# Kernel tuning notes

Hardware: AMD Instinct MI355X
Metric: run time of the kernel (lower is better)

Reference implementation:

```python
import jax, jax.numpy as jnp
import numpy as np

BATCH, E = 4096, 8
DIMS = [512, 1024, 1024, 512]


def setup_inputs() -> dict:
    key = jax.random.key(0)
    ks = jax.random.split(key, 8)
    inp = {
        'weight_blend': jax.random.uniform(ks[0], (BATCH, E), dtype=jnp.float32),
        'x': jax.random.normal(ks[1], (BATCH, DIMS[0]), dtype=jnp.float32),
    }
    for i in range(3):
        inp[f'W{i}'] = jax.random.normal(ks[2 + i], (E, DIMS[i + 1], DIMS[i]), dtype=jnp.float32)
        inp[f'B{i}'] = jnp.zeros((E, DIMS[i + 1]), dtype=jnp.float32)
    return inp


def _blended_layer(weight_blend, x, W, B):
    # Fused form of: weight = sum_e blend[b,e]*W[e]; y = bmm(weight, x) + sum_e blend[b,e]*B[e]
    # Computed as sum_e blend_e * (W_e @ x) without materializing (batch,out,in).
    y = jnp.einsum('eoi,bi->beo', W, x)          # per-expert GEMM, (B,E,out)
    y = jnp.einsum('be,beo->bo', weight_blend, y)  # blend combine
    return y + weight_blend @ B                   # blended bias (B,out)


def reference(weight_blend, x, W0, B0, W1, B1, W2, B2):
    # Dropout with keep_prob=0.0 is identity in eval mode; activations: elu, elu, linear.
    h = jax.nn.elu(_blended_layer(weight_blend, x, W0, B0))
    h = jax.nn.elu(_blended_layer(weight_blend, h, W1, B1))
    out = _blended_layer(weight_blend, h, W2, B2)
    return out
```

## Files before the change

kernel.cpp:

```cpp
#include <hip/hip_runtime.h>
#include <cstdint>
#include <cstddef>

typedef __bf16 bf16x8 __attribute__((ext_vector_type(8)));
typedef float f32x4 __attribute__((ext_vector_type(4)));
typedef unsigned short u16;
typedef unsigned short u16x8 __attribute__((ext_vector_type(8)));

#define BATCH 4096
#define NE 8

__device__ __forceinline__ u16 f2bf(float f) {
  union { float f; uint32_t u; } v; v.f = f;
  uint32_t u = v.u;
  u += 0x7fffu + ((u >> 16) & 1u);
  return (u16)(u >> 16);
}

__device__ __forceinline__ void cast8(const float* src, u16* dst) {
  const float4* p = (const float4*)src;
  float4 a = p[0], b = p[1];
  u16x8 o;
  o[0] = f2bf(a.x); o[1] = f2bf(a.y); o[2] = f2bf(a.z); o[3] = f2bf(a.w);
  o[4] = f2bf(b.x); o[5] = f2bf(b.y); o[6] = f2bf(b.z); o[7] = f2bf(b.w);
  *(u16x8*)dst = o;
}

__device__ __forceinline__ void conv_w_chunk(const float* __restrict__ W,
                                             u16* __restrict__ Bt,
                                             int N, int K0, int chunk) {
  int per_row = K0 >> 3;
  int rid = chunk / per_row;
  int i0 = (chunk - rid * per_row) << 3;
  int e = rid / N;
  int o = rid - e * N;
  cast8(W + (size_t)rid * K0 + i0,
        Bt + (size_t)o * ((size_t)NE * K0) + (size_t)e * K0 + i0);
}

__global__ void prep_kernel(const float* __restrict__ x,
                            const float* __restrict__ W0,
                            const float* __restrict__ W1,
                            const float* __restrict__ W2,
                            u16* __restrict__ h0, u16* __restrict__ Bt0,
                            u16* __restrict__ Bt1, u16* __restrict__ Bt2) {
  int t = blockIdx.x * blockDim.x + threadIdx.x;
  const int C0 = BATCH * 512 / 8;
  const int C1 = C0 + NE * 1024 * 512 / 8;
  const int C2 = C1 + NE * 1024 * 1024 / 8;
  if (t < C0) {
    cast8(x + (size_t)t * 8, h0 + (size_t)t * 8);
  } else if (t < C1) {
    conv_w_chunk(W0, Bt0, 1024, 512, t - C0);
  } else if (t < C2) {
    conv_w_chunk(W1, Bt1, 1024, 1024, t - C1);
  } else {
    conv_w_chunk(W2, Bt2, 512, 1024, t - C2);
  }
}

template<int SLICES, bool ELU_ACT, bool OUT_BF16>
__global__ void combine_kernel(const float* __restrict__ P,
                               const float* __restrict__ blend,
                               const float* __restrict__ Bias,
                               void* __restrict__ outp, int N) {
  int t = blockIdx.x * blockDim.x + threadIdx.x;
  int per_row = N >> 3;
  int b = t / per_row;
  int i0 = (t - b * per_row) << 3;
  const size_t slice = (size_t)BATCH * N;
  float v[8] = {0, 0, 0, 0, 0, 0, 0, 0};
  #pragma unroll
  for (int s = 0; s < SLICES; ++s) {
    const float4* p = (const float4*)(P + s * slice + (size_t)b * N + i0);
    float4 pa = p[0], pb = p[1];
    v[0] += pa.x; v[1] += pa.y; v[2] += pa.z; v[3] += pa.w;
    v[4] += pb.x; v[5] += pb.y; v[6] += pb.z; v[7] += pb.w;
  }
  const float4* blp = (const float4*)(blend + b * NE);
  float4 u0 = blp[0], u1 = blp[1];
  float bl[8] = {u0.x, u0.y, u0.z, u0.w, u1.x, u1.y, u1.z, u1.w};
  #pragma unroll
  for (int e = 0; e < NE; ++e) {
    const float4* bp = (const float4*)(Bias + (size_t)e * N + i0);
    float4 ba = bp[0], bb = bp[1];
    float bv[8] = {ba.x, ba.y, ba.z, ba.w, bb.x, bb.y, bb.z, bb.w};
    #pragma unroll
    for (int j = 0; j < 8; ++j) v[j] += bl[e] * bv[j];
  }
  if (ELU_ACT) {
    #pragma unroll
    for (int j = 0; j < 8; ++j) v[j] = v[j] > 0.f ? v[j] : expm1f(v[j]);
  }
  if (OUT_BF16) {
    u16x8 o;
    #pragma unroll
    for (int j = 0; j < 8; ++j) o[j] = f2bf(v[j]);
    *(u16x8*)((u16*)outp + (size_t)b * N + i0) = o;
  } else {
    float4* op = (float4*)((float*)outp + (size_t)b * N + i0);
    op[0] = (float4){v[0], v[1], v[2], v[3]};
    op[1] = (float4){v[4], v[5], v[6], v[7]};
  }
}

#define GL2LDS(g, l) __builtin_amdgcn_global_load_lds( \
    (__attribute__((address_space(1))) void*)(g),      \
    (__attribute__((address_space(3))) void*)(l), 16, 0, 0)

template<int K0, int NEXP>
__global__ __launch_bounds__(256, 2)
void gemm_hb_kernel(const u16* __restrict__ h, const u16* __restrict__ Bt,
                    const float* __restrict__ blend, float* __restrict__ P, int N) {
  __shared__ __align__(16) u16 Hs[128 * 32];
  __shared__ __align__(16) u16 Bs[128 * 32];
  __shared__ float bls[128 * NE];

  const int tid  = threadIdx.x;
  const int w    = tid >> 6, lane = tid & 63;
  const int wm   = w >> 1,   wn   = w & 1;
  const int lrow = lane & 15, quad = lane >> 4;

  const int row0 = blockIdx.x * 128;
  const int col0 = blockIdx.y * 128;
  const int EK = K0 * NE;
  const int e0 = blockIdx.z * NEXP;

  ((float4*)bls)[tid] = ((const float4*)(blend + (size_t)row0 * NE))[tid];

  const u16* gH0 = h + (size_t)(row0 + (tid >> 2)) * K0 + ((tid & 3) << 3);
  const u16* gH1 = gH0 + (size_t)64 * K0;
  const u16* gB0 = Bt + (size_t)(col0 + (tid >> 2)) * EK + (size_t)e0 * K0 + ((tid & 3) << 3);
  const u16* gB1 = gB0 + (size_t)64 * EK;
  u16* lH0 = &Hs[tid * 8];
  u16* lH1 = &Hs[tid * 8 + 2048];
  u16* lB0 = &Bs[tid * 8];
  u16* lB1 = &Bs[tid * 8 + 2048];

  const u16* fH[4];
  const u16* fB[4];
  #pragma unroll
  for (int i = 0; i < 4; ++i) {
    fH[i] = &Hs[(wm * 64 + i * 16 + lrow) * 32 + quad * 8];
    fB[i] = &Bs[(wn * 64 + i * 16 + lrow) * 32 + quad * 8];
  }

  f32x4 acc[4][4];
  #pragma unroll
  for (int i = 0; i < 4; ++i)
    #pragma unroll
    for (int j = 0; j < 4; ++j) acc[i][j] = (f32x4){0.f, 0.f, 0.f, 0.f};

  #pragma unroll
  for (int e = 0; e < NEXP; ++e) {
    f32x4 acc2[4][4];
    #pragma unroll
    for (int i = 0; i < 4; ++i)
      #pragma unroll
      for (int j = 0; j < 4; ++j) acc2[i][j] = (f32x4){0.f, 0.f, 0.f, 0.f};

    const u16* pH0 = gH0;
    const u16* pH1 = gH1;
    const u16* pB0 = gB0 + (size_t)e * K0;
    const u16* pB1 = gB1 + (size_t)e * K0;

    for (int it = 0; it < K0 / 32; ++it) {
      GL2LDS(pH0, lH0);
      GL2LDS(pH1, lH1);
      GL2LDS(pB0, lB0);
      GL2LDS(pB1, lB1);
      pH0 += 32; pH1 += 32; pB0 += 32; pB1 += 32;
      __syncthreads();

      bf16x8 hf[4], bfr[4];
      #pragma unroll
      for (int i = 0; i < 4; ++i) hf[i] = *(const bf16x8*)fH[i];
      #pragma unroll
      for (int j = 0; j < 4; ++j) bfr[j] = *(const bf16x8*)fB[j];
      #pragma unroll
      for (int i = 0; i < 4; ++i)
        #pragma unroll
        for (int j = 0; j < 4; ++j)
          acc2[i][j] = __builtin_amdgcn_mfma_f32_16x16x32_bf16(hf[i], bfr[j], acc2[i][j], 0, 0, 0);
      __syncthreads();
    }

    #pragma unroll
    for (int mt = 0; mt < 4; ++mt) {
      float bl[4];
      #pragma unroll
      for (int r = 0; r < 4; ++r)
        bl[r] = bls[(wm * 64 + mt * 16 + quad * 4 + r) * NE + (e0 + e)];
      #pragma unroll
      for (int nt = 0; nt < 4; ++nt)
        #pragma unroll
        for (int r = 0; r < 4; ++r)
          acc[mt][nt][r] += bl[r] * acc2[mt][nt][r];
    }
  }

  float* Ps = P + (size_t)blockIdx.z * ((size_t)BATCH * N);
  #pragma unroll
  for (int mt = 0; mt < 4; ++mt) {
    #pragma unroll
    for (int r = 0; r < 4; ++r) {
      int row = row0 + wm * 64 + mt * 16 + quad * 4 + r;
      #pragma unroll
      for (int nt = 0; nt < 4; ++nt) {
        int col = col0 + wn * 64 + nt * 16 + lrow;
        Ps[(size_t)row * N + col] = acc[mt][nt][r];
      }
    }
  }
}

extern "C" void kernel_launch(void* const* d_in, const int* in_sizes, int n_in,
                              void* d_out, int out_size, void* d_ws, size_t ws_size,
                              hipStream_t stream) {
  const float* blend = (const float*)d_in[0];
  const float* x  = (const float*)d_in[1];
  const float* W0 = (const float*)d_in[2];
  const float* B0 = (const float*)d_in[3];
  const float* W1 = (const float*)d_in[4];
  const float* B1 = (const float*)d_in[5];
  const float* W2 = (const float*)d_in[6];
  const float* B2 = (const float*)d_in[7];
  float* out = (float*)d_out;

  char* ws = (char*)d_ws;
  u16*   hA  = (u16*)ws;
  u16*   h1  = (u16*)(ws + 8388608);
  u16*   Bt0 = (u16*)(ws + 16777216);
  u16*   Bt1 = (u16*)(ws + 25165824);
  u16*   Bt2 = (u16*)(ws + 41943040);
  float* P   = (float*)(ws + 50331648);

  prep_kernel<<<9216, 256, 0, stream>>>(x, W0, W1, W2, hA, Bt0, Bt1, Bt2);

  gemm_hb_kernel<512, 2><<<dim3(32, 8, 4), 256, 0, stream>>>(hA, Bt0, blend, P, 1024);
  combine_kernel<4, true, true><<<2048, 256, 0, stream>>>(P, blend, B0, h1, 1024);

  gemm_hb_kernel<1024, 2><<<dim3(32, 8, 4), 256, 0, stream>>>(h1, Bt1, blend, P, 1024);
  combine_kernel<4, true, true><<<2048, 256, 0, stream>>>(P, blend, B1, hA, 1024);

  gemm_hb_kernel<1024, 1><<<dim3(32, 4, 8), 256, 0, stream>>>(hA, Bt2, blend, P, 512);
  combine_kernel<8, false, false><<<1024, 256, 0, stream>>>(P, blend, B2, out, 512);
}
```

Baseline: 355.4 us.

## Store per-expert GEMM outputs in bf16 and apply blend in combine kernel

```diff
diff --git a/kernel.cpp b/kernel.cpp
--- a/kernel.cpp
+++ b/kernel.cpp
@@ -15,6 +15,11 @@
   uint32_t u = v.u;
   u += 0x7fffu + ((u >> 16) & 1u);
   return (u16)(u >> 16);
+}
+
+__device__ __forceinline__ float bf2f(u16 u) {
+  union { uint32_t u; float f; } v; v.u = ((uint32_t)u) << 16;
+  return v.f;
 }
 
 __device__ __forceinline__ void cast8(const float* src, u16* dst) {
@@ -59,27 +64,26 @@
   }
 }
 
-template<int SLICES, bool ELU_ACT, bool OUT_BF16>
-__global__ void combine_kernel(const float* __restrict__ P,
-                               const float* __restrict__ blend,
-                               const float* __restrict__ Bias,
-                               void* __restrict__ outp, int N) {
+template<bool ELU_ACT, bool OUT_BF16>
+__global__ void combine8_kernel(const u16* __restrict__ P,
+                                const float* __restrict__ blend,
+                                const float* __restrict__ Bias,
+                                void* __restrict__ outp, int N) {
   int t = blockIdx.x * blockDim.x + threadIdx.x;
   int per_row = N >> 3;
   int b = t / per_row;
   int i0 = (t - b * per_row) << 3;
   const size_t slice = (size_t)BATCH * N;
-  float v[8] = {0, 0, 0, 0, 0, 0, 0, 0};
-  #pragma unroll
-  for (int s = 0; s < SLICES; ++s) {
-    const float4* p = (const float4*)(P + s * slice + (size_t)b * N + i0);
-    float4 pa = p[0], pb = p[1];
-    v[0] += pa.x; v[1] += pa.y; v[2] += pa.z; v[3] += pa.w;
-    v[4] += pb.x; v[5] += pb.y; v[6] += pb.z; v[7] += pb.w;
-  }
   const float4* blp = (const float4*)(blend + b * NE);
   float4 u0 = blp[0], u1 = blp[1];
   float bl[8] = {u0.x, u0.y, u0.z, u0.w, u1.x, u1.y, u1.z, u1.w};
+  float v[8] = {0, 0, 0, 0, 0, 0, 0, 0};
+  #pragma unroll
+  for (int e = 0; e < NE; ++e) {
+    u16x8 pv = *(const u16x8*)(P + (size_t)e * slice + (size_t)b * N + i0);
+    #pragma unroll
+    for (int j = 0; j < 8; ++j) v[j] += bl[e] * bf2f(pv[j]);
+  }
   #pragma unroll
   for (int e = 0; e < NE; ++e) {
     const float4* bp = (const float4*)(Bias + (size_t)e * N + i0);
@@ -108,13 +112,12 @@
     (__attribute__((address_space(1))) void*)(g),      \
     (__attribute__((address_space(3))) void*)(l), 16, 0, 0)
 
-template<int K0, int NEXP>
-__global__ __launch_bounds__(256, 2)
-void gemm_hb_kernel(const u16* __restrict__ h, const u16* __restrict__ Bt,
-                    const float* __restrict__ blend, float* __restrict__ P, int N) {
+template<int K0>
+__global__ __launch_bounds__(256, 4)
+void gemm_be_kernel(const u16* __restrict__ h, const u16* __restrict__ Bt,
+                    u16* __restrict__ P, int N) {
   __shared__ __align__(16) u16 Hs[128 * 32];
   __shared__ __align__(16) u16 Bs[128 * 32];
-  __shared__ float bls[128 * NE];
 
   const int tid  = threadIdx.x;
   const int w    = tid >> 6, lane = tid & 63;
@@ -123,14 +126,12 @@
 
   const int row0 = blockIdx.x * 128;
   const int col0 = blockIdx.y * 128;
-  const int EK = K0 * NE;
-  const int e0 = blockIdx.z * NEXP;
-
-  ((float4*)bls)[tid] = ((const float4*)(blend + (size_t)row0 * NE))[tid];
+  const int e    = blockIdx.z;
+  const int EK   = K0 * NE;
 
   const u16* gH0 = h + (size_t)(row0 + (tid >> 2)) * K0 + ((tid & 3) << 3);
   const u16* gH1 = gH0 + (size_t)64 * K0;
-  const u16* gB0 = Bt + (size_t)(col0 + (tid >> 2)) * EK + (size_t)e0 * K0 + ((tid & 3) << 3);
+  const u16* gB0 = Bt + (size_t)(col0 + (tid >> 2)) * EK + (size_t)e * K0 + ((tid & 3) << 3);
   const u16* gB1 = gB0 + (size_t)64 * EK;
   u16* lH0 = &Hs[tid * 8];
   u16* lH1 = &Hs[tid * 8 + 2048];
@@ -151,55 +152,28 @@
     #pragma unroll
     for (int j = 0; j < 4; ++j) acc[i][j] = (f32x4){0.f, 0.f, 0.f, 0.f};
 
-  #pragma unroll
-  for (int e = 0; e < NEXP; ++e) {
-    f32x4 acc2[4][4];
+  for (int it = 0; it < K0 / 32; ++it) {
+    GL2LDS(gH0, lH0);
+    GL2LDS(gH1, lH1);
+    GL2LDS(gB0, lB0);
+    GL2LDS(gB1, lB1);
+    gH0 += 32; gH1 += 32; gB0 += 32; gB1 += 32;
+    __syncthreads();
+
+    bf16x8 hf[4], bfr[4];
+    #pragma unroll
+    for (int i = 0; i < 4; ++i) hf[i] = *(const bf16x8*)fH[i];
+    #pragma unroll
+    for (int j = 0; j < 4; ++j) bfr[j] = *(const bf16x8*)fB[j];
     #pragma unroll
     for (int i = 0; i < 4; ++i)
       #pragma unroll
-      for (int j = 0; j < 4; ++j) acc2[i][j] = (f32x4){0.f, 0.f, 0.f, 0.f};
-
-    const u16* pH0 = gH0;
-    const u16* pH1 = gH1;
-    const u16* pB0 = gB0 + (size_t)e * K0;
-    const u16* pB1 = gB1 + (size_t)e * K0;
-
-    for (int it = 0; it < K0 / 32; ++it) {
-      GL2LDS(pH0, lH0);
-      GL2LDS(pH1, lH1);
-      GL2LDS(pB0, lB0);
-      GL2LDS(pB1, lB1);
-      pH0 += 32; pH1 += 32; pB0 += 32; pB1 += 32;
-      __syncthreads();
-
-      bf16x8 hf[4], bfr[4];
-      #pragma unroll
-      for (int i = 0; i < 4; ++i) hf[i] = *(const bf16x8*)fH[i];
-      #pragma unroll
-      for (int j = 0; j < 4; ++j) bfr[j] = *(const bf16x8*)fB[j];
-      #pragma unroll
-      for (int i = 0; i < 4; ++i)
-        #pragma unroll
-        for (int j = 0; j < 4; ++j)
-          acc2[i][j] = __builtin_amdgcn_mfma_f32_16x16x32_bf16(hf[i], bfr[j], acc2[i][j], 0, 0, 0);
-      __syncthreads();
-    }
-
-    #pragma unroll
-    for (int mt = 0; mt < 4; ++mt) {
-      float bl[4];
-      #pragma unroll
-      for (int r = 0; r < 4; ++r)
-        bl[r] = bls[(wm * 64 + mt * 16 + quad * 4 + r) * NE + (e0 + e)];
-      #pragma unroll
-      for (int nt = 0; nt < 4; ++nt)
-        #pragma unroll
-        for (int r = 0; r < 4; ++r)
-          acc[mt][nt][r] += bl[r] * acc2[mt][nt][r];
-    }
-  }
-
-  float* Ps = P + (size_t)blockIdx.z * ((size_t)BATCH * N);
+      for (int j = 0; j < 4; ++j)
+        acc[i][j] = __builtin_amdgcn_mfma_f32_16x16x32_bf16(hf[i], bfr[j], acc[i][j], 0, 0, 0);
+    __syncthreads();
+  }
+
+  u16* Ps = P + (size_t)e * ((size_t)BATCH * N);
   #pragma unroll
   for (int mt = 0; mt < 4; ++mt) {
     #pragma unroll
@@ -208,7 +182,7 @@
       #pragma unroll
       for (int nt = 0; nt < 4; ++nt) {
         int col = col0 + wn * 64 + nt * 16 + lrow;
-        Ps[(size_t)row * N + col] = acc[mt][nt][r];
+        Ps[(size_t)row * N + col] = f2bf(acc[mt][nt][r]);
       }
     }
   }
@@ -228,21 +202,21 @@
   float* out = (float*)d_out;
 
   char* ws = (char*)d_ws;
-  u16*   hA  = (u16*)ws;
-  u16*   h1  = (u16*)(ws + 8388608);
-  u16*   Bt0 = (u16*)(ws + 16777216);
-  u16*   Bt1 = (u16*)(ws + 25165824);
-  u16*   Bt2 = (u16*)(ws + 41943040);
-  float* P   = (float*)(ws + 50331648);
+  u16* hA  = (u16*)ws;
+  u16* h1  = (u16*)(ws + 8388608);
+  u16* Bt0 = (u16*)(ws + 16777216);
+  u16* Bt1 = (u16*)(ws + 25165824);
+  u16* Bt2 = (u16*)(ws + 41943040);
+  u16* P   = (u16*)(ws + 50331648);
 
   prep_kernel<<<9216, 256, 0, stream>>>(x, W0, W1, W2, hA, Bt0, Bt1, Bt2);
 
-  gemm_hb_kernel<512, 2><<<dim3(32, 8, 4), 256, 0, stream>>>(hA, Bt0, blend, P, 1024);
-  combine_kernel<4, true, true><<<2048, 256, 0, stream>>>(P, blend, B0, h1, 1024);
-
-  gemm_hb_kernel<1024, 2><<<dim3(32, 8, 4), 256, 0, stream>>>(h1, Bt1, blend, P, 1024);
-  combine_kernel<4, true, true><<<2048, 256, 0, stream>>>(P, blend, B1, hA, 1024);
-
-  gemm_hb_kernel<1024, 1><<<dim3(32, 4, 8), 256, 0, stream>>>(hA, Bt2, blend, P, 512);
-  combine_kernel<8, false, false><<<1024, 256, 0, stream>>>(P, blend, B2, out, 512);
-}
+  gemm_be_kernel<512><<<dim3(32, 8, 8), 256, 0, stream>>>(hA, Bt0, P, 1024);
+  combine8_kernel<true, true><<<2048, 256, 0, stream>>>(P, blend, B0, h1, 1024);
+
+  gemm_be_kernel<1024><<<dim3(32, 8, 8), 256, 0, stream>>>(h1, Bt1, P, 1024);
+  combine8_kernel<true, true><<<2048, 256, 0, stream>>>(P, blend, B1, hA, 1024);
+
+  gemm_be_kernel<1024><<<dim3(32, 4, 8), 256, 0, stream>>>(hA, Bt2, P, 512);
+  combine8_kernel<false, false><<<1024, 256, 0, stream>>>(P, blend, B2, out, 512);
+}
```

After: 323.2 us. -9.1%, faster.
